# Optimization experiments

Hardware: AMD Instinct MI355X
Metric: run time of the kernel (lower is better)

Reference implementation:

```python
import jax, jax.numpy as jnp
import numpy as np

B, S, D, H = 4, 2048, 1024, 16
DH = D // H  # head dim == module's 'scale'


def setup_inputs() -> dict:
    key = jax.random.key(0)
    ks = jax.random.split(key, 9)
    std = 1.0 / np.sqrt(D)
    return {
        "x": jax.random.normal(ks[0], (B, S, D), dtype=jnp.float32),
        "Wq": jax.random.normal(ks[1], (D, D), dtype=jnp.float32) * std,
        "bq": jax.random.normal(ks[2], (D,), dtype=jnp.float32) * std,
        "Wk": jax.random.normal(ks[3], (D, D), dtype=jnp.float32) * std,
        "bk": jax.random.normal(ks[4], (D,), dtype=jnp.float32) * std,
        "Wv": jax.random.normal(ks[5], (D, D), dtype=jnp.float32) * std,
        "bv": jax.random.normal(ks[6], (D,), dtype=jnp.float32) * std,
        "Wo": jax.random.normal(ks[7], (D, D), dtype=jnp.float32) * std,
        "bo": jax.random.normal(ks[8], (D,), dtype=jnp.float32) * std,
    }


def reference(x, Wq, bq, Wk, bk, Wv, bv, Wo, bo):
    b, s, d = x.shape
    # torch Linear: y = x @ W.T + b
    q = (x @ Wq.T + bq).reshape(b, s, H, DH).transpose(0, 2, 1, 3)  # [B,H,S,Dh]
    k = (x @ Wk.T + bk).reshape(b, s, H, DH).transpose(0, 2, 1, 3)
    v = (x @ Wv.T + bv).reshape(b, s, H, DH).transpose(0, 2, 1, 3)
    # scaled dot-product with causal mask (prefill: Tq == Tk, empty cache)
    scores = jnp.einsum("bhqd,bhkd->bhqk", q, k) / jnp.sqrt(
        jnp.asarray(DH, dtype=jnp.float32))
    causal = jnp.tril(jnp.ones((s, s), dtype=bool))  # [S,S]
    scores = jnp.where(causal, scores, jnp.asarray(-1e9, dtype=scores.dtype))
    attn = jax.nn.softmax(scores, axis=-1)
    out = jnp.einsum("bhqk,bhkd->bhqd", attn, v)  # [B,H,S,Dh]
    out = out.transpose(0, 2, 1, 3).reshape(b, s, d)
    return out @ Wo.T + bo
```

## Files before the change

kernel.cpp:

```cpp
#include <hip/hip_runtime.h>
#include <hip/hip_bf16.h>
#include <stdint.h>

#define NB 4
#define NS 2048
#define ND 1024
#define NH 16
#define NDH 64
#define NM (NB*NS)

typedef __attribute__((ext_vector_type(8))) short bf16x8;
typedef __attribute__((ext_vector_type(4))) float f32x4;
typedef __attribute__((ext_vector_type(16))) float f32x16;
typedef __attribute__((ext_vector_type(8))) unsigned short u16x8;

static __device__ __forceinline__ unsigned short f2bf(float f) {
  union { float f; unsigned u; } v; v.f = f;
  return (unsigned short)((v.u + 0x7FFFu + ((v.u >> 16) & 1u)) >> 16);
}

static __device__ __forceinline__ void gload_lds16(const void* g, void* l) {
  __builtin_amdgcn_global_load_lds(
      (__attribute__((address_space(1))) unsigned int*)(uintptr_t)g,
      (__attribute__((address_space(3))) unsigned int*)(uintptr_t)(size_t)(l),
      16, 0, 0);
}

static __device__ __forceinline__ unsigned cvtpk(float lo, float hi) {
  unsigned r;
  asm("v_cvt_pk_bf16_f32 %0, %1, %2" : "=v"(r) : "v"(lo), "v"(hi));
  return r;
}
static __device__ __forceinline__ void plswap(unsigned &a, unsigned &b) {
  asm("v_permlane32_swap_b32 %0, %1" : "+v"(a), "+v"(b));
}

__global__ void k_cvt(const float* __restrict__ src, unsigned short* __restrict__ dst, int n8) {
  int i = blockIdx.x * blockDim.x + threadIdx.x;
  if (i >= n8) return;
  const float4* s = (const float4*)src + (size_t)i * 2;
  float4 a = s[0], b = s[1];
  u16x8 o;
  o[0]=f2bf(a.x); o[1]=f2bf(a.y); o[2]=f2bf(a.z); o[3]=f2bf(a.w);
  o[4]=f2bf(b.x); o[5]=f2bf(b.y); o[6]=f2bf(b.z); o[7]=f2bf(b.w);
  *((u16x8*)dst + i) = o;
}

__global__ void k_cvtw(const float* __restrict__ s0, const float* __restrict__ s1,
                       const float* __restrict__ s2, const float* __restrict__ s3,
                       unsigned short* __restrict__ d0, unsigned short* __restrict__ d1,
                       unsigned short* __restrict__ d2, unsigned short* __restrict__ d3) {
  constexpr int NG = ND*ND/8;
  int i = blockIdx.x * blockDim.x + threadIdx.x;
  const int m = i / NG, j = i - m*NG;
  const float* src = m==0 ? s0 : (m==1 ? s1 : (m==2 ? s2 : s3));
  unsigned short* dst = m==0 ? d0 : (m==1 ? d1 : (m==2 ? d2 : d3));
  const float4* s = (const float4*)src + (size_t)j * 2;
  float4 a = s[0], b = s[1];
  u16x8 o;
  o[0]=f2bf(a.x); o[1]=f2bf(a.y); o[2]=f2bf(a.z); o[3]=f2bf(a.w);
  o[4]=f2bf(b.x); o[5]=f2bf(b.y); o[6]=f2bf(b.z); o[7]=f2bf(b.w);
  *((u16x8*)dst + j) = o;
}

__global__ __launch_bounds__(256)
void k_gemm_qkv(const unsigned short* __restrict__ A,
                const unsigned short* __restrict__ Wqp, const unsigned short* __restrict__ Wkp,
                const unsigned short* __restrict__ Wvp,
                const float* __restrict__ bqp, const float* __restrict__ bkp,
                const float* __restrict__ bvp,
                unsigned short* __restrict__ Qo, unsigned short* __restrict__ Ko,
                unsigned short* __restrict__ Vto, float qscale)
{
  constexpr int K = ND, BK = 32;
  __shared__ unsigned short Alds[128*BK];
  __shared__ unsigned short Blds[128*BK];
  const int bcf = blockIdx.x;
  const int mat = bcf >> 3, bc = bcf & 7;
  const unsigned short* W = mat==0 ? Wqp : (mat==1 ? Wkp : Wvp);
  const float* bias = mat==0 ? bqp : (mat==1 ? bkp : bvp);
  const float scale = mat==0 ? qscale : 1.0f;

  const int tid = threadIdx.x;
  const int wid = tid >> 6, lane = tid & 63;
  const int g = lane >> 4, lr = lane & 15;
  const int br = blockIdx.y;
  const int wr = (wid >> 1) << 6, wc = (wid & 1) << 6;

  f32x4 acc[4][4];
  #pragma unroll
  for (int m=0;m<4;m++)
    #pragma unroll
    for (int n=0;n<4;n++) acc[m][n] = f32x4{0.f,0.f,0.f,0.f};

  const unsigned short* Ab = A + (size_t)br*128*K;
  const unsigned short* Wb = W + (size_t)bc*128*K;
  const int r0 = tid >> 2, c0 = (tid & 3) * 8;
  const int r1 = (256 + tid) >> 2;

  for (int k0 = 0; k0 < K; k0 += BK) {
    gload_lds16(Ab + (size_t)r0*K + k0 + c0, &Alds[tid*8]);
    gload_lds16(Ab + (size_t)r1*K + k0 + c0, &Alds[(256+tid)*8]);
    gload_lds16(Wb + (size_t)r0*K + k0 + c0, &Blds[tid*8]);
    gload_lds16(Wb + (size_t)r1*K + k0 + c0, &Blds[(256+tid)*8]);
    __syncthreads();
    bf16x8 af[4], bfr[4];
    #pragma unroll
    for (int m=0;m<4;m++) af[m]  = *(const bf16x8*)&Alds[(wr + m*16 + lr)*BK + g*8];
    #pragma unroll
    for (int n=0;n<4;n++) bfr[n] = *(const bf16x8*)&Blds[(wc + n*16 + lr)*BK + g*8];
    #pragma unroll
    for (int m=0;m<4;m++)
      #pragma unroll
      for (int n=0;n<4;n++)
        acc[m][n] = __builtin_amdgcn_mfma_f32_16x16x32_bf16(af[m], bfr[n], acc[m][n], 0, 0, 0);
    __syncthreads();
  }

  #pragma unroll
  for (int m=0;m<4;m++) {
    const int rbase = br*128 + wr + m*16 + g*4;
    #pragma unroll
    for (int n=0;n<4;n++) {
      const int col = bc*128 + wc + n*16 + lr;
      const float bv = bias[col];
      #pragma unroll
      for (int j=0;j<4;j++) {
        const int row = rbase + j;
        const float val = (acc[m][n][j] + bv) * scale;
        const int b = row >> 11, s = row & (NS-1), h = col >> 6, dh = col & 63;
        if (mat == 2)
          Vto[(((size_t)b*NH + h)*NDH + dh)*NS + s] = f2bf(val);
        else
          (mat==0 ? Qo : Ko)[(((size_t)b*NH + h)*NS + s)*NDH + dh] = f2bf(val);
      }
    }
  }
}

__global__ __launch_bounds__(256)
void k_gemm_o(const unsigned short* __restrict__ A,
              const unsigned short* __restrict__ W,
              const float* __restrict__ bias,
              float* __restrict__ outp)
{
  constexpr int K = ND, BK = 32;
  __shared__ unsigned short Alds[128*BK];
  __shared__ unsigned short Blds[128*BK];
  const int tid = threadIdx.x;
  const int wid = tid >> 6, lane = tid & 63;
  const int g = lane >> 4, lr = lane & 15;
  const int bc = blockIdx.x, br = blockIdx.y;
  const int wr = (wid >> 1) << 6, wc = (wid & 1) << 6;

  f32x4 acc[4][4];
  #pragma unroll
  for (int m=0;m<4;m++)
    #pragma unroll
    for (int n=0;n<4;n++) acc[m][n] = f32x4{0.f,0.f,0.f,0.f};

  const unsigned short* Ab = A + (size_t)br*128*K;
  const unsigned short* Wb = W + (size_t)bc*128*K;
  const int r0 = tid >> 2, c0 = (tid & 3) * 8;
  const int r1 = (256 + tid) >> 2;

  for (int k0 = 0; k0 < K; k0 += BK) {
    gload_lds16(Ab + (size_t)r0*K + k0 + c0, &Alds[tid*8]);
    gload_lds16(Ab + (size_t)r1*K + k0 + c0, &Alds[(256+tid)*8]);
    gload_lds16(Wb + (size_t)r0*K + k0 + c0, &Blds[tid*8]);
    gload_lds16(Wb + (size_t)r1*K + k0 + c0, &Blds[(256+tid)*8]);
    __syncthreads();
    bf16x8 af[4], bfr[4];
    #pragma unroll
    for (int m=0;m<4;m++) af[m]  = *(const bf16x8*)&Alds[(wr + m*16 + lr)*BK + g*8];
    #pragma unroll
    for (int n=0;n<4;n++) bfr[n] = *(const bf16x8*)&Blds[(wc + n*16 + lr)*BK + g*8];
    #pragma unroll
    for (int m=0;m<4;m++)
      #pragma unroll
      for (int n=0;n<4;n++)
        acc[m][n] = __builtin_amdgcn_mfma_f32_16x16x32_bf16(af[m], bfr[n], acc[m][n], 0, 0, 0);
    __syncthreads();
  }

  #pragma unroll
  for (int m=0;m<4;m++) {
    const int rbase = br*128 + wr + m*16 + g*4;
    #pragma unroll
    for (int n=0;n<4;n++) {
      const int col = bc*128 + wc + n*16 + lr;
      const float bv = bias[col];
      #pragma unroll
      for (int j=0;j<4;j++)
        outp[(size_t)(rbase + j)*ND + col] = acc[m][n][j] + bv;
    }
  }
}

__global__ __launch_bounds__(128, 4)
void k_attn(const unsigned short* __restrict__ Qg,
            const unsigned short* __restrict__ Kg,
            const unsigned short* __restrict__ Vtg,
            unsigned short* __restrict__ Og)
{
  __shared__ unsigned short Klds[64*64];
  __shared__ unsigned short Vlds[64*64];
  __shared__ float scL[64];
  const int tid = threadIdx.x;
  const int wid = tid >> 6, lane = tid & 63;
  const int ql = lane & 31, hi = lane >> 5;
  const int bh = blockIdx.x;
  const int qt = (int)gridDim.y - 1 - (int)blockIdx.y;
  const int qbB = qt * 64;
  const int wq = qbB + wid * 32;

  const unsigned short* Qh  = Qg  + (size_t)bh*NS*NDH;
  const unsigned short* Kh  = Kg  + (size_t)bh*NS*NDH;
  const unsigned short* Vth = Vtg + (size_t)bh*NDH*NS;

  bf16x8 qf[4];
  #pragma unroll
  for (int ds=0; ds<4; ++ds)
    qf[ds] = *(const bf16x8*)(Qh + (size_t)(wq+ql)*NDH + ds*16 + hi*8);

  f32x16 acc0, acc1;
  #pragma unroll
  for (int r=0;r<16;++r) { acc0[r]=0.f; acc1[r]=0.f; }
  float lsum = 0.f;

  const int sr = tid >> 3, sc = tid & 7;
  const int swz = (sc ^ (sr & 7)) * 8;

  const int ntiles = qt + 1;
  for (int kt = 0; kt < ntiles; ++kt) {
    const int kbase = kt << 6;
    #pragma unroll
    for (int c=0;c<4;c++)
      gload_lds16(Kh + (size_t)(kbase + c*16 + sr)*NDH + swz, &Klds[(c*128+tid)*8]);
    #pragma unroll
    for (int c=0;c<4;c++)
      gload_lds16(Vth + (size_t)(c*16 + sr)*NS + kbase + swz, &Vlds[(c*128+tid)*8]);
    __syncthreads();
    #pragma unroll
    for (int h32 = 0; h32 < 2; ++h32) {
      const int kb32 = kbase + h32*32;
      if (kb32 <= wq) {
        const int krow = h32*32 + ql;
        f32x16 st;
        #pragma unroll
        for (int r=0;r<16;++r) st[r] = 0.f;
        __builtin_amdgcn_s_setprio(1);
        #pragma unroll
        for (int ds=0; ds<4; ++ds) {
          bf16x8 kf = *(const bf16x8*)&Klds[krow*64 + (((ds*2+hi) ^ (krow&7))*8)];
          st = __builtin_amdgcn_mfma_f32_32x32x16_bf16(kf, qf[ds], st, 0,0,0);
        }
        __builtin_amdgcn_s_setprio(0);
        if (kb32 == wq) {
          #pragma unroll
          for (int r=0;r<16;++r) {
            const int koff = (r&3) + 8*(r>>2) + 4*hi;
            if (koff > ql) st[r] = -1e30f;
          }
        }
        float p[16]; float ls = 0.f;
        #pragma unroll
        for (int r=0;r<16;++r) { p[r] = __builtin_amdgcn_exp2f(st[r]); ls += p[r]; }
        lsum += ls;
        unsigned w0 = cvtpk(p[0],p[1]),  w1 = cvtpk(p[2],p[3]);
        unsigned w2 = cvtpk(p[4],p[5]),  w3 = cvtpk(p[6],p[7]);
        plswap(w0, w2); plswap(w1, w3);
        unsigned z0 = cvtpk(p[8],p[9]),  z1 = cvtpk(p[10],p[11]);
        unsigned z2 = cvtpk(p[12],p[13]),z3 = cvtpk(p[14],p[15]);
        plswap(z0, z2); plswap(z1, z3);
        union { unsigned u[4]; bf16x8 v; } pk0, pk1;
        pk0.u[0]=w0; pk0.u[1]=w1; pk0.u[2]=w2; pk0.u[3]=w3;
        pk1.u[0]=z0; pk1.u[1]=z1; pk1.u[2]=z2; pk1.u[3]=z3;
        __builtin_amdgcn_s_setprio(1);
        #pragma unroll
        for (int nt=0; nt<2; ++nt) {
          const int drow = nt*32 + ql;
          #pragma unroll
          for (int ksl=0; ksl<2; ++ksl) {
            const int slot = h32*4 + ksl*2 + hi;
            bf16x8 vf = *(const bf16x8*)&Vlds[drow*64 + ((slot ^ (drow&7))*8)];
            f32x16 &a = nt ? acc1 : acc0;
            a = __builtin_amdgcn_mfma_f32_32x32x16_bf16(ksl ? pk1.v : pk0.v, vf, a, 0,0,0);
          }
        }
        __builtin_amdgcn_s_setprio(0);
      }
    }
    __syncthreads();
  }

  const float l = lsum + __shfl_xor(lsum, 32, 64);
  scL[wid*32 + ql] = 1.0f / l;
  const int b = bh >> 4, h = bh & 15;
  #pragma unroll
  for (int rq=0; rq<4; ++rq) {
    f32x4 lv = *(const f32x4*)&scL[wid*32 + rq*8 + 4*hi];
    #pragma unroll
    for (int j=0;j<4;j++) {
      const float inv = lv[j];
      const int s = wq + rq*8 + 4*hi + j;
      unsigned short* orow = Og + ((size_t)b*NS + s)*ND + h*NDH;
      orow[ql]      = f2bf(acc0[rq*4+j] * inv);
      orow[32 + ql] = f2bf(acc1[rq*4+j] * inv);
    }
  }
}

extern "C" void kernel_launch(void* const* d_in, const int* in_sizes, int n_in,
                              void* d_out, int out_size, void* d_ws, size_t ws_size,
                              hipStream_t stream) {
  (void)in_sizes; (void)n_in; (void)out_size; (void)ws_size;
  const float* x  = (const float*)d_in[0];
  const float* Wq = (const float*)d_in[1];
  const float* bq = (const float*)d_in[2];
  const float* Wk = (const float*)d_in[3];
  const float* bk = (const float*)d_in[4];
  const float* Wv = (const float*)d_in[5];
  const float* bv = (const float*)d_in[6];
  const float* Wo = (const float*)d_in[7];
  const float* bo = (const float*)d_in[8];

  char* ws = (char*)d_ws;
  unsigned short* xb  = (unsigned short*)(ws + 0);
  unsigned short* Wqb = (unsigned short*)(ws + 16777216);
  unsigned short* Wkb = (unsigned short*)(ws + 18874368);
  unsigned short* Wvb = (unsigned short*)(ws + 20971520);
  unsigned short* Wob = (unsigned short*)(ws + 23068672);
  unsigned short* Qb  = (unsigned short*)(ws + 25165824);
  unsigned short* Kb  = (unsigned short*)(ws + 41943040);
  unsigned short* Vtb = (unsigned short*)(ws + 58720256);
  unsigned short* Ob  = (unsigned short*)(ws + 75497472);

  k_cvt<<<dim3(NM*ND/8/256), dim3(256), 0, stream>>>(x, xb, NM*ND/8);
  k_cvtw<<<dim3(4*ND*ND/8/256), dim3(256), 0, stream>>>(Wq, Wk, Wv, Wo, Wqb, Wkb, Wvb, Wob);

  const float qscale = 0.125f * 1.4426950408889634f;
  k_gemm_qkv<<<dim3(24, NM/128), dim3(256), 0, stream>>>(
      xb, Wqb, Wkb, Wvb, bq, bk, bv, Qb, Kb, Vtb, qscale);

  k_attn<<<dim3(NB*NH, NS/64), dim3(128), 0, stream>>>(Qb, Kb, Vtb, Ob);

  k_gemm_o<<<dim3(ND/128, NM/128), dim3(256), 0, stream>>>(Ob, Wob, bo, (float*)d_out);
}
```

Measured before the change: 184.6 us.

## Fuse conversion kernels, double-buffer QKV GEMM, enlarge attention query tile

Merges the activation and weight bf16 conversion launches into one kernel. Double-buffers the QKV GEMM LDS tiles so the next K slice loads while MFMAs run, with one barrier per step instead of two, and raises MFMA priority. Attention blocks grow to 256 threads covering 128 query rows with 4 waves sharing each K/V tile, halving redundant K/V loads but coarsening causal load balance. Launch bounds are also tightened for occupancy.

```diff
diff --git a/kernel.cpp b/kernel.cpp
--- a/kernel.cpp
+++ b/kernel.cpp
@@ -35,26 +35,23 @@
   asm("v_permlane32_swap_b32 %0, %1" : "+v"(a), "+v"(b));
 }
 
-__global__ void k_cvt(const float* __restrict__ src, unsigned short* __restrict__ dst, int n8) {
+__global__ void k_cvt_all(const float* __restrict__ x,
+                          const float* __restrict__ s0, const float* __restrict__ s1,
+                          const float* __restrict__ s2, const float* __restrict__ s3,
+                          unsigned short* __restrict__ xd,
+                          unsigned short* __restrict__ d0, unsigned short* __restrict__ d1,
+                          unsigned short* __restrict__ d2, unsigned short* __restrict__ d3) {
+  constexpr int NGX = NM*ND/8;
+  constexpr int NGW = ND*ND/8;
   int i = blockIdx.x * blockDim.x + threadIdx.x;
-  if (i >= n8) return;
-  const float4* s = (const float4*)src + (size_t)i * 2;
-  float4 a = s[0], b = s[1];
-  u16x8 o;
-  o[0]=f2bf(a.x); o[1]=f2bf(a.y); o[2]=f2bf(a.z); o[3]=f2bf(a.w);
-  o[4]=f2bf(b.x); o[5]=f2bf(b.y); o[6]=f2bf(b.z); o[7]=f2bf(b.w);
-  *((u16x8*)dst + i) = o;
-}
-
-__global__ void k_cvtw(const float* __restrict__ s0, const float* __restrict__ s1,
-                       const float* __restrict__ s2, const float* __restrict__ s3,
-                       unsigned short* __restrict__ d0, unsigned short* __restrict__ d1,
-                       unsigned short* __restrict__ d2, unsigned short* __restrict__ d3) {
-  constexpr int NG = ND*ND/8;
-  int i = blockIdx.x * blockDim.x + threadIdx.x;
-  const int m = i / NG, j = i - m*NG;
-  const float* src = m==0 ? s0 : (m==1 ? s1 : (m==2 ? s2 : s3));
-  unsigned short* dst = m==0 ? d0 : (m==1 ? d1 : (m==2 ? d2 : d3));
+  const float* src; unsigned short* dst; int j;
+  if (i < NGX) { src = x; dst = xd; j = i; }
+  else {
+    const int k = i - NGX, m = k / NGW;
+    j = k - m*NGW;
+    src = m==0 ? s0 : (m==1 ? s1 : (m==2 ? s2 : s3));
+    dst = m==0 ? d0 : (m==1 ? d1 : (m==2 ? d2 : d3));
+  }
   const float4* s = (const float4*)src + (size_t)j * 2;
   float4 a = s[0], b = s[1];
   u16x8 o;
@@ -63,7 +60,7 @@
   *((u16x8*)dst + j) = o;
 }
 
-__global__ __launch_bounds__(256)
+__global__ __launch_bounds__(256, 4)
 void k_gemm_qkv(const unsigned short* __restrict__ A,
                 const unsigned short* __restrict__ Wqp, const unsigned short* __restrict__ Wkp,
                 const unsigned short* __restrict__ Wvp,
@@ -73,8 +70,8 @@
                 unsigned short* __restrict__ Vto, float qscale)
 {
   constexpr int K = ND, BK = 32;
-  __shared__ unsigned short Alds[128*BK];
-  __shared__ unsigned short Blds[128*BK];
+  __shared__ unsigned short Alds[2][128*BK];
+  __shared__ unsigned short Blds[2][128*BK];
   const int bcf = blockIdx.x;
   const int mat = bcf >> 3, bc = bcf & 7;
   const unsigned short* W = mat==0 ? Wqp : (mat==1 ? Wkp : Wvp);
@@ -98,23 +95,32 @@
   const int r0 = tid >> 2, c0 = (tid & 3) * 8;
   const int r1 = (256 + tid) >> 2;
 
+  auto stage = [&](int b, int k0) {
+    gload_lds16(Ab + (size_t)r0*K + k0 + c0, &Alds[b][tid*8]);
+    gload_lds16(Ab + (size_t)r1*K + k0 + c0, &Alds[b][(256+tid)*8]);
+    gload_lds16(Wb + (size_t)r0*K + k0 + c0, &Blds[b][tid*8]);
+    gload_lds16(Wb + (size_t)r1*K + k0 + c0, &Blds[b][(256+tid)*8]);
+  };
+
+  stage(0, 0);
+  __syncthreads();
+  int cur = 0;
   for (int k0 = 0; k0 < K; k0 += BK) {
-    gload_lds16(Ab + (size_t)r0*K + k0 + c0, &Alds[tid*8]);
-    gload_lds16(Ab + (size_t)r1*K + k0 + c0, &Alds[(256+tid)*8]);
-    gload_lds16(Wb + (size_t)r0*K + k0 + c0, &Blds[tid*8]);
-    gload_lds16(Wb + (size_t)r1*K + k0 + c0, &Blds[(256+tid)*8]);
-    __syncthreads();
+    if (k0 + BK < K) stage(cur ^ 1, k0 + BK);
     bf16x8 af[4], bfr[4];
     #pragma unroll
-    for (int m=0;m<4;m++) af[m]  = *(const bf16x8*)&Alds[(wr + m*16 + lr)*BK + g*8];
-    #pragma unroll
-    for (int n=0;n<4;n++) bfr[n] = *(const bf16x8*)&Blds[(wc + n*16 + lr)*BK + g*8];
+    for (int m=0;m<4;m++) af[m]  = *(const bf16x8*)&Alds[cur][(wr + m*16 + lr)*BK + g*8];
+    #pragma unroll
+    for (int n=0;n<4;n++) bfr[n] = *(const bf16x8*)&Blds[cur][(wc + n*16 + lr)*BK + g*8];
+    __builtin_amdgcn_s_setprio(1);
     #pragma unroll
     for (int m=0;m<4;m++)
       #pragma unroll
       for (int n=0;n<4;n++)
         acc[m][n] = __builtin_amdgcn_mfma_f32_16x16x32_bf16(af[m], bfr[n], acc[m][n], 0, 0, 0);
-    __syncthreads();
+    __builtin_amdgcn_s_setprio(0);
+    __syncthreads();
+    cur ^= 1;
   }
 
   #pragma unroll
@@ -138,7 +144,7 @@
   }
 }
 
-__global__ __launch_bounds__(256)
+__global__ __launch_bounds__(256, 4)
 void k_gemm_o(const unsigned short* __restrict__ A,
               const unsigned short* __restrict__ W,
               const float* __restrict__ bias,
@@ -197,7 +203,7 @@
   }
 }
 
-__global__ __launch_bounds__(128, 4)
+__global__ __launch_bounds__(256, 4)
 void k_attn(const unsigned short* __restrict__ Qg,
             const unsigned short* __restrict__ Kg,
             const unsigned short* __restrict__ Vtg,
@@ -205,13 +211,13 @@
 {
   __shared__ unsigned short Klds[64*64];
   __shared__ unsigned short Vlds[64*64];
-  __shared__ float scL[64];
+  __shared__ float scL[128];
   const int tid = threadIdx.x;
   const int wid = tid >> 6, lane = tid & 63;
   const int ql = lane & 31, hi = lane >> 5;
   const int bh = blockIdx.x;
   const int qt = (int)gridDim.y - 1 - (int)blockIdx.y;
-  const int qbB = qt * 64;
+  const int qbB = qt * 128;
   const int wq = qbB + wid * 32;
 
   const unsigned short* Qh  = Qg  + (size_t)bh*NS*NDH;
@@ -231,15 +237,15 @@
   const int sr = tid >> 3, sc = tid & 7;
   const int swz = (sc ^ (sr & 7)) * 8;
 
-  const int ntiles = qt + 1;
+  const int ntiles = 2*qt + 2;
   for (int kt = 0; kt < ntiles; ++kt) {
     const int kbase = kt << 6;
     #pragma unroll
-    for (int c=0;c<4;c++)
-      gload_lds16(Kh + (size_t)(kbase + c*16 + sr)*NDH + swz, &Klds[(c*128+tid)*8]);
-    #pragma unroll
-    for (int c=0;c<4;c++)
-      gload_lds16(Vth + (size_t)(c*16 + sr)*NS + kbase + swz, &Vlds[(c*128+tid)*8]);
+    for (int c=0;c<2;c++)
+      gload_lds16(Kh + (size_t)(kbase + c*32 + sr)*NDH + swz, &Klds[(c*256+tid)*8]);
+    #pragma unroll
+    for (int c=0;c<2;c++)
+      gload_lds16(Vth + (size_t)(c*32 + sr)*NS + kbase + swz, &Vlds[(c*256+tid)*8]);
     __syncthreads();
     #pragma unroll
     for (int h32 = 0; h32 < 2; ++h32) {
@@ -336,14 +342,15 @@
   unsigned short* Vtb = (unsigned short*)(ws + 58720256);
   unsigned short* Ob  = (unsigned short*)(ws + 75497472);
 
-  k_cvt<<<dim3(NM*ND/8/256), dim3(256), 0, stream>>>(x, xb, NM*ND/8);
-  k_cvtw<<<dim3(4*ND*ND/8/256), dim3(256), 0, stream>>>(Wq, Wk, Wv, Wo, Wqb, Wkb, Wvb, Wob);
+  constexpr int CVT_BLOCKS = (NM*ND/8 + 4*ND*ND/8) / 256;
+  k_cvt_all<<<dim3(CVT_BLOCKS), dim3(256), 0, stream>>>(
+      x, Wq, Wk, Wv, Wo, xb, Wqb, Wkb, Wvb, Wob);
 
   const float qscale = 0.125f * 1.4426950408889634f;
   k_gemm_qkv<<<dim3(24, NM/128), dim3(256), 0, stream>>>(
       xb, Wqb, Wkb, Wvb, bq, bk, bv, Qb, Kb, Vtb, qscale);
 
-  k_attn<<<dim3(NB*NH, NS/64), dim3(128), 0, stream>>>(Qb, Kb, Vtb, Ob);
+  k_attn<<<dim3(NB*NH, NS/128), dim3(256), 0, stream>>>(Qb, Kb, Vtb, Ob);
 
   k_gemm_o<<<dim3(ND/128, NM/128), dim3(256), 0, stream>>>(Ob, Wob, bo, (float*)d_out);
 }
```

Result: faster. 179.7 us (-2.6%).
